# Performance work log

Measured on AMD Instinct MI355X. Metric: run time of the kernel, lower is better.

The kernel has to match this reference:

```python
import jax, jax.numpy as jnp
import numpy as np

HID = 4096; NH = 32; NKV = 8; HD = 128; EPS = 1e-6; BASE = 10000.0

def _rmsnorm(x, w):
    # RMSNorm over last (head_dim) axis
    return x * jax.lax.rsqrt(jnp.mean(x * x, axis=-1, keepdims=True) + EPS) * w

def _rope(x, positions):
    # neox-style rotary on (b, s, h, HD): rotate halves
    half = HD // 2
    inv_freq = 1.0 / (BASE ** (jnp.arange(0, HD, 2, dtype=jnp.float32) / HD))  # (half,)
    ang = positions.astype(jnp.float32)[:, None] * inv_freq                    # (s, half)
    cos = jnp.cos(ang)[None, :, None, :]
    sin = jnp.sin(ang)[None, :, None, :]
    x1, x2 = x[..., :half], x[..., half:]
    return jnp.concatenate([x1 * cos - x2 * sin, x2 * cos + x1 * sin], axis=-1)

def setup_inputs() -> dict:
    key = jax.random.key(0)
    k0, k1, k2 = jax.random.split(key, 3)
    b, s = 4, 1024
    return {
        "h_shard": jax.random.normal(k0, (b, s, HID), jnp.float32),
        "positions": jnp.arange(s, dtype=jnp.int32),
        "w_qkv": jax.random.normal(k1, (NH * HD + 2 * NKV * HD, HID), jnp.float32) * 0.02,
        "w_o": jax.random.normal(k2, (HID, NH * HD), jnp.float32) * 0.02,
        "q_norm_w": jnp.ones((HD,), jnp.float32),
        "k_norm_w": jnp.ones((HD,), jnp.float32),
    }

def reference(h_shard, positions, w_qkv, w_o, q_norm_w, k_norm_w):
    b, s, _ = h_shard.shape
    q_sz, kv_sz = NH * HD, NKV * HD
    # fused QKV projection (world_size=1 -> ag_mm is a plain matmul x @ W.T)
    qkv = h_shard @ w_qkv.T                                   # (b, s, q_sz + 2*kv_sz)
    q = qkv[..., :q_sz].reshape(b, s, NH, HD)
    k = qkv[..., q_sz:q_sz + kv_sz].reshape(b, s, NKV, HD)
    v = qkv[..., q_sz + kv_sz:].reshape(b, s, NKV, HD)
    # per-head RMSNorm then RoPE on q/k (Qwen3 ordering)
    q = _rope(_rmsnorm(q, q_norm_w), positions)
    k = _rope(_rmsnorm(k, k_norm_w), positions)
    # GQA SDPA without materializing repeated KV: group query heads per kv head
    g = NH // NKV
    qg = q.reshape(b, s, NKV, g, HD)
    scores = jnp.einsum('bskgd,btkd->bkgst', qg, k) / jnp.sqrt(jnp.float32(HD))
    causal = jnp.tril(jnp.ones((s, s), dtype=bool))
    scores = jnp.where(causal, scores, -jnp.inf)
    probs = jax.nn.softmax(scores, axis=-1)
    attn = jnp.einsum('bkgst,btkd->bskgd', probs, v).reshape(b, s, q_sz)
    # output projection (mm_rs -> plain matmul for world_size=1)
    return attn @ w_o.T
```

## Files before the change

kernel.cpp:

```cpp
#include <hip/hip_runtime.h>

typedef __bf16 bf16;
typedef __bf16 bf16x4 __attribute__((ext_vector_type(4)));
typedef __bf16 bf16x8 __attribute__((ext_vector_type(8)));
typedef float f32x4 __attribute__((ext_vector_type(4)));

#define HID 4096
#define QKV_N 6144
#define NTOK 4096

#define BAR() __builtin_amdgcn_s_barrier()

__device__ __forceinline__ void gload_lds16(const bf16* g, bf16* l) {
  __builtin_amdgcn_global_load_lds(
      (__attribute__((address_space(1))) void*)(g),
      (__attribute__((address_space(3))) void*)(l), 16, 0, 0);
}

__global__ void cvt_kernel(const float4* __restrict__ s, bf16x4* __restrict__ d) {
  int i = blockIdx.x * blockDim.x + threadIdx.x;
  float4 v = s[i];
  bf16x4 o;
  o[0] = (bf16)v.x; o[1] = (bf16)v.y; o[2] = (bf16)v.z; o[3] = (bf16)v.w;
  d[i] = o;
}

template <typename OutT>
__global__ __launch_bounds__(256) void gemm_bt(
    const bf16* __restrict__ A, const bf16* __restrict__ Bm,
    OutT* __restrict__ C, int M, int N, int K)
{
  __shared__ bf16 As[128 * 64];
  __shared__ bf16 Bs[128 * 64];
  const int tid = threadIdx.x;
  const int w = tid >> 6, l = tid & 63;
  const int quad = l >> 4, lane16 = l & 15;
  const int row0 = blockIdx.y * 128, col0 = blockIdx.x * 128;
  const int wm = (w & 1) * 64, wn = (w >> 1) * 64;
  const int lrow = l >> 3;
  const int lkswz = ((l & 7) ^ lrow) * 8;
  const int sw = lane16 & 7;

  f32x4 acc[4][4];
#pragma unroll
  for (int a = 0; a < 4; ++a)
#pragma unroll
    for (int b = 0; b < 4; ++b) acc[a][b] = (f32x4){0.f, 0.f, 0.f, 0.f};

  for (int k0 = 0; k0 < K; k0 += 64) {
#pragma unroll
    for (int r = 0; r < 4; ++r) {
      int i = r * 4 + w;
      gload_lds16(A + (size_t)(row0 + i * 8 + lrow) * K + k0 + lkswz, &As[i * 512 + l * 8]);
      gload_lds16(Bm + (size_t)(col0 + i * 8 + lrow) * K + k0 + lkswz, &Bs[i * 512 + l * 8]);
    }
    __syncthreads();
#pragma unroll
    for (int kk = 0; kk < 2; ++kk) {
      bf16x8 af[4], bfr[4];
#pragma unroll
      for (int im = 0; im < 4; ++im)
        af[im] = *(const bf16x8*)&As[(wm + im * 16 + lane16) * 64 + (((kk * 4 + quad) ^ sw) * 8)];
#pragma unroll
      for (int in_ = 0; in_ < 4; ++in_)
        bfr[in_] = *(const bf16x8*)&Bs[(wn + in_ * 16 + lane16) * 64 + (((kk * 4 + quad) ^ sw) * 8)];
#pragma unroll
      for (int im = 0; im < 4; ++im)
#pragma unroll
        for (int in_ = 0; in_ < 4; ++in_)
          acc[im][in_] = __builtin_amdgcn_mfma_f32_16x16x32_bf16(af[im], bfr[in_], acc[im][in_], 0, 0, 0);
    }
    __syncthreads();
  }
#pragma unroll
  for (int im = 0; im < 4; ++im) {
#pragma unroll
    for (int r = 0; r < 4; ++r) {
      int row = row0 + wm + im * 16 + quad * 4 + r;
      OutT* cp = C + (size_t)row * N + col0 + wn;
#pragma unroll
      for (int in_ = 0; in_ < 4; ++in_)
        cp[in_ * 16 + lane16] = (OutT)acc[im][in_][r];
    }
  }
}

template <typename OutT>
__global__ __launch_bounds__(512, 2) void gemm_bt256(
    const bf16* __restrict__ A, const bf16* __restrict__ Bm,
    OutT* __restrict__ C, int M, int N, int K)
{
  __shared__ __align__(16) bf16 As[2][256 * 64];
  __shared__ __align__(16) bf16 Bs[2][256 * 64];

  const int tid = threadIdx.x;
  const int w = tid >> 6, l = tid & 63;
  const int quad = l >> 4, lane16 = l & 15;
  const int sw = lane16 & 7;
  const int lrow = l >> 3;
  const int lk = (l & 7) ^ lrow;

  const int nwg = gridDim.x * gridDim.y;
  int bid = blockIdx.y * gridDim.x + blockIdx.x;
  bid = (bid & 7) * (nwg >> 3) + (bid >> 3);
  const int row0 = (bid / gridDim.x) * 256;
  const int col0 = (bid % gridDim.x) * 256;

  const int wm = (w >> 2) * 64;
  const int wn = (w & 3) * 32;

  f32x4 acc[2][2][4][2];
#pragma unroll
  for (int mq = 0; mq < 2; ++mq)
#pragma unroll
    for (int nq = 0; nq < 2; ++nq)
#pragma unroll
      for (int im = 0; im < 4; ++im)
#pragma unroll
        for (int in_ = 0; in_ < 2; ++in_) acc[mq][nq][im][in_] = (f32x4){0.f, 0.f, 0.f, 0.f};

  bf16x8 aF0[4][2], aF1[4][2];
  bf16x8 bF0[2][2], bF1[2][2];

  auto stA = [&](int buf, int half, int kt) {
    const bf16* g = A + (size_t)(row0 + half * 128 + w * 8 + lrow) * K + kt * 64 + lk * 8;
    bf16* s = &As[buf][(half * 128 + w * 8) * 64 + l * 8];
    gload_lds16(g, s);
    gload_lds16(g + (size_t)64 * K, s + 64 * 64);
  };
  auto stB = [&](int buf, int half, int kt) {
    const bf16* g = Bm + (size_t)(col0 + half * 128 + w * 8 + lrow) * K + kt * 64 + lk * 8;
    bf16* s = &Bs[buf][(half * 128 + w * 8) * 64 + l * 8];
    gload_lds16(g, s);
    gload_lds16(g + (size_t)64 * K, s + 64 * 64);
  };

  auto loadAF = [&](const bf16* Ap, bf16x8 (&dst)[4][2], int mq) {
#pragma unroll
    for (int im = 0; im < 4; ++im)
#pragma unroll
      for (int kk = 0; kk < 2; ++kk)
        dst[im][kk] = *(const bf16x8*)&Ap[(mq * 128 + wm + im * 16 + lane16) * 64 +
                                          (((kk * 4 + quad) ^ sw) * 8)];
  };
  auto loadBF = [&](const bf16* Bp, bf16x8 (&dst)[2][2], int nq) {
#pragma unroll
    for (int in_ = 0; in_ < 2; ++in_)
#pragma unroll
      for (int kk = 0; kk < 2; ++kk)
        dst[in_][kk] = *(const bf16x8*)&Bp[(nq * 128 + wn + in_ * 16 + lane16) * 64 +
                                           (((kk * 4 + quad) ^ sw) * 8)];
  };
  auto mma = [&](bf16x8 (&a)[4][2], bf16x8 (&b)[2][2], f32x4 (&ac)[4][2]) {
#pragma unroll
    for (int im = 0; im < 4; ++im)
#pragma unroll
      for (int in_ = 0; in_ < 2; ++in_) {
        ac[im][in_] = __builtin_amdgcn_mfma_f32_16x16x32_bf16(a[im][0], b[in_][0], ac[im][in_], 0, 0, 0);
        ac[im][in_] = __builtin_amdgcn_mfma_f32_16x16x32_bf16(a[im][1], b[in_][1], ac[im][in_], 0, 0, 0);
      }
  };

  const int nt = K >> 6;

  stA(0, 0, 0); stB(0, 0, 0); stB(0, 1, 0); stA(0, 1, 0);
  stA(1, 0, 1); stB(1, 0, 1); stB(1, 1, 1); stA(1, 1, 1);
  asm volatile("s_waitcnt vmcnt(12)" ::: "memory");
  BAR();
  loadAF(As[0], aF0, 0);
  asm volatile("s_waitcnt lgkmcnt(0)" ::: "memory");
  BAR();

  for (int t = 0; t < nt; ++t) {
    const int p = t & 1;
    const bf16* Ap = As[p];
    const bf16* Bp = Bs[p];
    const int kt = (t + 2 < nt) ? (t + 2) : (nt - 1);

    loadBF(Bp, bF0, 0);
    stA(p, 0, kt);
    BAR();
    asm volatile("s_waitcnt lgkmcnt(0)" ::: "memory");
    __builtin_amdgcn_s_setprio(1);
    mma(aF0, bF0, acc[0][0]);
    __builtin_amdgcn_s_setprio(0);
    asm volatile("s_waitcnt vmcnt(4)" ::: "memory");
    BAR();

    loadBF(Bp, bF1, 1);
    stB(p, 0, kt);
    BAR();
    asm volatile("s_waitcnt lgkmcnt(0)" ::: "memory");
    __builtin_amdgcn_s_setprio(1);
    mma(aF0, bF1, acc[0][1]);
    __builtin_amdgcn_s_setprio(0);
    asm volatile("s_waitcnt vmcnt(4)" ::: "memory");
    BAR();

    loadAF(Ap, aF1, 1);
    stB(p, 1, kt);
    BAR();
    asm volatile("s_waitcnt lgkmcnt(0)" ::: "memory");
    __builtin_amdgcn_s_setprio(1);
    mma(aF1, bF1, acc[1][1]);
    __builtin_amdgcn_s_setprio(0);
    asm volatile("s_waitcnt vmcnt(4)" ::: "memory");
    BAR();

    if (t + 1 < nt) loadAF(As[p ^ 1], aF0, 0);
    stA(p, 1, kt);
    BAR();
    __builtin_amdgcn_s_setprio(1);
    mma(aF1, bF0, acc[1][0]);
    __builtin_amdgcn_s_setprio(0);
    asm volatile("s_waitcnt vmcnt(4) lgkmcnt(0)" ::: "memory");
    BAR();
  }

#pragma unroll
  for (int mq = 0; mq < 2; ++mq)
#pragma unroll
    for (int im = 0; im < 4; ++im)
#pragma unroll
      for (int r = 0; r < 4; ++r) {
        int row = row0 + mq * 128 + wm + im * 16 + quad * 4 + r;
        OutT* cp = C + (size_t)row * N + col0 + wn;
#pragma unroll
        for (int nq = 0; nq < 2; ++nq)
#pragma unroll
          for (int in_ = 0; in_ < 2; ++in_)
            cp[nq * 128 + in_ * 16 + lane16] = (OutT)acc[mq][nq][im][in_][r];
      }
}

__global__ __launch_bounds__(256) void norm_rope_kernel(
    bf16* __restrict__ qkv, const int* __restrict__ pos,
    const float* __restrict__ qw, const float* __restrict__ kw)
{
  int g = blockIdx.x * 4 + (threadIdx.x >> 6);
  int tok = g / 40;
  int slot = g % 40;
  int d = threadIdx.x & 63;
  bf16* base;
  const float* w;
  if (slot < 32) { base = qkv + (size_t)tok * QKV_N + slot * 128; w = qw; }
  else           { base = qkv + (size_t)tok * QKV_N + HID + (slot - 32) * 128; w = kw; }
  float x1 = (float)base[d], x2 = (float)base[d + 64];
  float ss = x1 * x1 + x2 * x2;
#pragma unroll
  for (int m = 1; m < 64; m <<= 1) ss += __shfl_xor(ss, m, 64);
  float rn = rsqrtf(ss * (1.0f / 128.0f) + 1e-6f);
  x1 = x1 * rn * w[d];
  x2 = x2 * rn * w[d + 64];
  int p = pos[tok & 1023];
  float invf = exp2f(-0.20762050593045952f * (float)d);
  float ang = (float)p * invf;
  float sn, c;
  sincosf(ang, &sn, &c);
  base[d]      = (bf16)(x1 * c - x2 * sn);
  base[d + 64] = (bf16)(x2 * c + x1 * sn);
}

__global__ __launch_bounds__(256) void flash_kernel(
    const bf16* __restrict__ qkv, bf16* __restrict__ attn)
{
  __shared__ bf16 Ks[2][64 * 128];
  __shared__ bf16 Vt[2][128 * 64];
  __shared__ bf16 Ps[4][16 * 72];

  const int bh = blockIdx.y;
  const int qt = ((bh >> 4) & 1) ? (15 - blockIdx.x) : blockIdx.x;
  const int batch = bh >> 5;
  const int qh = bh & 31;
  const int kvh = qh >> 2;
  const int tid = threadIdx.x;
  const int w = tid >> 6, l = tid & 63;
  const int quad = l >> 4, lane16 = l & 15;
  const int sw = lane16 & 7;
  const size_t tok0 = (size_t)batch * 1024;
  const int q0 = qt * 64;

  bf16x8 qf[4];
  {
    const bf16* qrow = qkv + (tok0 + q0 + w * 16 + lane16) * QKV_N + qh * 128 + quad * 8;
#pragma unroll
    for (int kk = 0; kk < 4; ++kk) qf[kk] = *(const bf16x8*)(qrow + kk * 32);
  }

  f32x4 O[8];
#pragma unroll
  for (int id = 0; id < 8; ++id) O[id] = (f32x4){0.f, 0.f, 0.f, 0.f};
  float l_run[4];
#pragma unroll
  for (int r = 0; r < 4; ++r) l_run[r] = 0.f;

  const float scale = 0.08838834764831845f;
  const float SMAX = 12.0f;
  bf16x8 vreg[4];

  auto stage_K = [&](int j, int buf) {
#pragma unroll
    for (int r = 0; r < 4; ++r) {
      int i = r * 4 + w;
      int rloc = i * 4 + (l >> 4);
      int o = (l & 15) ^ (rloc & 7);
      const bf16* g = qkv + (tok0 + j * 64 + rloc) * QKV_N + HID + kvh * 128 + o * 8;
      gload_lds16(g, &Ks[buf][i * 512 + l * 8]);
    }
  };
  auto load_V = [&](int j) {
#pragma unroll
    for (int c = 0; c < 4; ++c) {
      int d0 = (c * 4 + w) * 8;
      vreg[c] = *(const bf16x8*)(qkv + (tok0 + j * 64 + l) * QKV_N + HID + 1024 + kvh * 128 + d0);
    }
  };
  auto write_V = [&](int buf) {
#pragma unroll
    for (int c = 0; c < 4; ++c) {
      int d0 = (c * 4 + w) * 8;
#pragma unroll
      for (int e = 0; e < 8; ++e) {
        int d = d0 + e;
        Vt[buf][d * 64 + (((l >> 3) ^ (d & 7)) * 8) + (l & 7)] = vreg[c][e];
      }
    }
  };

  stage_K(0, 0);
  load_V(0);
  write_V(0);
  __syncthreads();

  for (int j = 0; j <= qt; ++j) {
    const int p = j & 1;
    if (j < qt) { stage_K(j + 1, p ^ 1); load_V(j + 1); }

    f32x4 s[4];
#pragma unroll
    for (int in_ = 0; in_ < 4; ++in_) s[in_] = (f32x4){0.f, 0.f, 0.f, 0.f};
#pragma unroll
    for (int kk = 0; kk < 4; ++kk) {
#pragma unroll
      for (int in_ = 0; in_ < 4; ++in_) {
        bf16x8 b = *(const bf16x8*)&Ks[p][(in_ * 16 + lane16) * 128 + (((kk * 4 + quad) ^ sw) * 8)];
        s[in_] = __builtin_amdgcn_mfma_f32_16x16x32_bf16(qf[kk], b, s[in_], 0, 0, 0);
      }
    }

    if (j < qt) write_V(p ^ 1);

    const bool edge = (j == qt);
#pragma unroll
    for (int r = 0; r < 4; ++r) {
      float rs = 0.f;
#pragma unroll
      for (int in_ = 0; in_ < 4; ++in_) {
        float v = s[in_][r] * scale;
        if (edge) {
          int t_abs = j * 64 + in_ * 16 + lane16;
          int q_abs = q0 + w * 16 + quad * 4 + r;
          v = (t_abs <= q_abs) ? v : -1e30f;
        }
        float pv = __expf(v - SMAX);
        rs += pv;
        Ps[w][(quad * 4 + r) * 72 + in_ * 16 + lane16] = (bf16)pv;
      }
      l_run[r] += rs;
    }

#pragma unroll
    for (int kt = 0; kt < 2; ++kt) {
      bf16x8 a = *(const bf16x8*)&Ps[w][lane16 * 72 + kt * 32 + quad * 8];
#pragma unroll
      for (int id = 0; id < 8; ++id) {
        bf16x8 b = *(const bf16x8*)&Vt[p][(id * 16 + lane16) * 64 + (((kt * 4 + quad) ^ sw) * 8)];
        O[id] = __builtin_amdgcn_mfma_f32_16x16x32_bf16(a, b, O[id], 0, 0, 0);
      }
    }
    __syncthreads();
  }

#pragma unroll
  for (int r = 0; r < 4; ++r) {
    float lsum = l_run[r];
#pragma unroll
    for (int m = 1; m < 16; m <<= 1) lsum += __shfl_xor(lsum, m, 64);
    float inv = 1.0f / lsum;
    int row = q0 + w * 16 + quad * 4 + r;
    bf16* orow = attn + (tok0 + row) * (size_t)HID + qh * 128;
#pragma unroll
    for (int id = 0; id < 8; ++id) orow[id * 16 + lane16] = (bf16)(O[id][r] * inv);
  }
}

extern "C" void kernel_launch(void* const* d_in, const int* in_sizes, int n_in,
                              void* d_out, int out_size, void* d_ws, size_t ws_size,
                              hipStream_t stream) {
  const float* h    = (const float*)d_in[0];
  const int*   pos  = (const int*)d_in[1];
  const float* wqkv = (const float*)d_in[2];
  const float* wo   = (const float*)d_in[3];
  const float* qw   = (const float*)d_in[4];
  const float* kw   = (const float*)d_in[5];
  float* out = (float*)d_out;

  bf16* hb    = (bf16*)d_ws;
  bf16* wqkvb = hb + 16777216;
  bf16* wob   = wqkvb + 25165824;
  bf16* qkvb  = wob + 16777216;
  bf16* attnb = qkvb + 25165824;

  cvt_kernel<<<16384, 256, 0, stream>>>((const float4*)h, (bf16x4*)hb);
  cvt_kernel<<<24576, 256, 0, stream>>>((const float4*)wqkv, (bf16x4*)wqkvb);
  cvt_kernel<<<16384, 256, 0, stream>>>((const float4*)wo, (bf16x4*)wob);

  gemm_bt<bf16><<<dim3(48, 32), 256, 0, stream>>>(hb, wqkvb, qkvb, NTOK, QKV_N, HID);

  norm_rope_kernel<<<NTOK * 40 / 4, 256, 0, stream>>>(qkvb, pos, qw, kw);

  flash_kernel<<<dim3(16, 128), 256, 0, stream>>>(qkvb, attnb);

  gemm_bt256<float><<<dim3(16, 16), 512, 0, stream>>>(attnb, wob, out, NTOK, HID, HID);
}
```

Measured before the change: 744.4 us.

## Halve flash KV tile to 32 for occupancy and split QKV GEMM across tile kernels

The flash attention kernel now processes 32-token KV tiles instead of 64, which halves the shared memory for K, V and P. It adds a launch bound of 3 blocks per CU and replaces the swizzled V transpose with a padded stride-40 layout. Separately, the QKV projection is split: the first 4096 output columns go through the 256-wide GEMM kernel and the remaining 2048 through the smaller-tile GEMM. The aim is more resident flash blocks and better GEMM tile efficiency, at the cost of twice as many loop iterations and barriers per query tile in attention.

Measured after the change: 727.4 us. 1.02x faster.

```diff
diff --git a/kernel.cpp b/kernel.cpp
--- a/kernel.cpp
+++ b/kernel.cpp
@@ -261,12 +261,12 @@
   base[d + 64] = (bf16)(x2 * c + x1 * sn);
 }
 
-__global__ __launch_bounds__(256) void flash_kernel(
+__global__ __launch_bounds__(256, 3) void flash_kernel(
     const bf16* __restrict__ qkv, bf16* __restrict__ attn)
 {
-  __shared__ bf16 Ks[2][64 * 128];
-  __shared__ bf16 Vt[2][128 * 64];
-  __shared__ bf16 Ps[4][16 * 72];
+  __shared__ __align__(16) bf16 Ks[2][32 * 128];
+  __shared__ __align__(16) bf16 Vt[2][128 * 40];
+  __shared__ __align__(16) bf16 Ps[4][16 * 40];
 
   const int bh = blockIdx.y;
   const int qt = ((bh >> 4) & 1) ? (15 - blockIdx.x) : blockIdx.x;
@@ -279,6 +279,7 @@
   const int sw = lane16 & 7;
   const size_t tok0 = (size_t)batch * 1024;
   const int q0 = qt * 64;
+  const int vtok = l & 31;
 
   bf16x8 qf[4];
   {
@@ -296,34 +297,32 @@
 
   const float scale = 0.08838834764831845f;
   const float SMAX = 12.0f;
-  bf16x8 vreg[4];
-
-  auto stage_K = [&](int j, int buf) {
-#pragma unroll
-    for (int r = 0; r < 4; ++r) {
+  bf16x8 vreg[2];
+
+  auto stage_K = [&](int j2, int buf) {
+#pragma unroll
+    for (int r = 0; r < 2; ++r) {
       int i = r * 4 + w;
-      int rloc = i * 4 + (l >> 4);
-      int o = (l & 15) ^ (rloc & 7);
-      const bf16* g = qkv + (tok0 + j * 64 + rloc) * QKV_N + HID + kvh * 128 + o * 8;
+      int rloc = i * 4 + quad;
+      int o = lane16 ^ (rloc & 7);
+      const bf16* g = qkv + (tok0 + j2 * 32 + rloc) * QKV_N + HID + kvh * 128 + o * 8;
       gload_lds16(g, &Ks[buf][i * 512 + l * 8]);
     }
   };
-  auto load_V = [&](int j) {
-#pragma unroll
-    for (int c = 0; c < 4; ++c) {
-      int d0 = (c * 4 + w) * 8;
-      vreg[c] = *(const bf16x8*)(qkv + (tok0 + j * 64 + l) * QKV_N + HID + 1024 + kvh * 128 + d0);
+  auto load_V = [&](int j2) {
+#pragma unroll
+    for (int c = 0; c < 2; ++c) {
+      int d0 = (l >> 5) * 64 + (c * 4 + w) * 8;
+      vreg[c] = *(const bf16x8*)(qkv + (tok0 + j2 * 32 + vtok) * QKV_N + HID + 1024 + kvh * 128 + d0);
     }
   };
   auto write_V = [&](int buf) {
 #pragma unroll
-    for (int c = 0; c < 4; ++c) {
-      int d0 = (c * 4 + w) * 8;
-#pragma unroll
-      for (int e = 0; e < 8; ++e) {
-        int d = d0 + e;
-        Vt[buf][d * 64 + (((l >> 3) ^ (d & 7)) * 8) + (l & 7)] = vreg[c][e];
-      }
+    for (int c = 0; c < 2; ++c) {
+      int d0 = (l >> 5) * 64 + (c * 4 + w) * 8;
+#pragma unroll
+      for (int e = 0; e < 8; ++e)
+        Vt[buf][(d0 + e) * 40 + vtok] = vreg[c][e];
     }
   };
 
@@ -332,49 +331,49 @@
   write_V(0);
   __syncthreads();
 
-  for (int j = 0; j <= qt; ++j) {
-    const int p = j & 1;
-    if (j < qt) { stage_K(j + 1, p ^ 1); load_V(j + 1); }
-
-    f32x4 s[4];
-#pragma unroll
-    for (int in_ = 0; in_ < 4; ++in_) s[in_] = (f32x4){0.f, 0.f, 0.f, 0.f};
+  const int last = 2 * qt + 1;
+  for (int j2 = 0; j2 <= last; ++j2) {
+    const int p = j2 & 1;
+    if (j2 < last) { stage_K(j2 + 1, p ^ 1); load_V(j2 + 1); }
+
+    f32x4 s[2];
+#pragma unroll
+    for (int in_ = 0; in_ < 2; ++in_) s[in_] = (f32x4){0.f, 0.f, 0.f, 0.f};
 #pragma unroll
     for (int kk = 0; kk < 4; ++kk) {
 #pragma unroll
-      for (int in_ = 0; in_ < 4; ++in_) {
+      for (int in_ = 0; in_ < 2; ++in_) {
         bf16x8 b = *(const bf16x8*)&Ks[p][(in_ * 16 + lane16) * 128 + (((kk * 4 + quad) ^ sw) * 8)];
         s[in_] = __builtin_amdgcn_mfma_f32_16x16x32_bf16(qf[kk], b, s[in_], 0, 0, 0);
       }
     }
 
-    if (j < qt) write_V(p ^ 1);
-
-    const bool edge = (j == qt);
+    if (j2 < last) write_V(p ^ 1);
+
+    const bool edge = (j2 >= 2 * qt);
 #pragma unroll
     for (int r = 0; r < 4; ++r) {
       float rs = 0.f;
 #pragma unroll
-      for (int in_ = 0; in_ < 4; ++in_) {
+      for (int in_ = 0; in_ < 2; ++in_) {
         float v = s[in_][r] * scale;
         if (edge) {
-          int t_abs = j * 64 + in_ * 16 + lane16;
+          int t_abs = j2 * 32 + in_ * 16 + lane16;
           int q_abs = q0 + w * 16 + quad * 4 + r;
           v = (t_abs <= q_abs) ? v : -1e30f;
         }
         float pv = __expf(v - SMAX);
         rs += pv;
-        Ps[w][(quad * 4 + r) * 72 + in_ * 16 + lane16] = (bf16)pv;
+        Ps[w][(quad * 4 + r) * 40 + in_ * 16 + lane16] = (bf16)pv;
       }
       l_run[r] += rs;
     }
 
-#pragma unroll
-    for (int kt = 0; kt < 2; ++kt) {
-      bf16x8 a = *(const bf16x8*)&Ps[w][lane16 * 72 + kt * 32 + quad * 8];
+    {
+      bf16x8 a = *(const bf16x8*)&Ps[w][lane16 * 40 + quad * 8];
 #pragma unroll
       for (int id = 0; id < 8; ++id) {
-        bf16x8 b = *(const bf16x8*)&Vt[p][(id * 16 + lane16) * 64 + (((kt * 4 + quad) ^ sw) * 8)];
+        bf16x8 b = *(const bf16x8*)&Vt[p][(id * 16 + lane16) * 40 + quad * 8];
         O[id] = __builtin_amdgcn_mfma_f32_16x16x32_bf16(a, b, O[id], 0, 0, 0);
       }
     }
@@ -415,7 +414,9 @@
   cvt_kernel<<<24576, 256, 0, stream>>>((const float4*)wqkv, (bf16x4*)wqkvb);
   cvt_kernel<<<16384, 256, 0, stream>>>((const float4*)wo, (bf16x4*)wob);
 
-  gemm_bt<bf16><<<dim3(48, 32), 256, 0, stream>>>(hb, wqkvb, qkvb, NTOK, QKV_N, HID);
+  gemm_bt256<bf16><<<dim3(16, 16), 512, 0, stream>>>(hb, wqkvb, qkvb, NTOK, QKV_N, HID);
+  gemm_bt<bf16><<<dim3(16, 32), 256, 0, stream>>>(
+      hb, wqkvb + (size_t)4096 * HID, qkvb + 4096, NTOK, QKV_N, HID);
 
   norm_rope_kernel<<<NTOK * 40 / 4, 256, 0, stream>>>(qkvb, pos, qw, kw);
 
```
